# Kernel tuning notes

Measured on AMD Instinct MI355X. Metric: run time of the kernel, lower is better.

Reference implementation:

```python
import jax, jax.numpy as jnp
import numpy as np

N, DIN, DOUT = 8192, 512, 256


def setup_inputs() -> dict:
    key = jax.random.key(0)
    ks = jax.random.split(key, 8)
    s_in = 1.0 / np.sqrt(DIN)   # ~ torch Linear default init scale
    s_out = 1.0 / np.sqrt(DOUT)
    return {
        "x": jax.random.normal(ks[0], (N, DIN), jnp.float32),
        "Wm": jax.random.normal(ks[1], (DIN, DOUT), jnp.float32) * s_in,
        "Wn": jax.random.normal(ks[2], (DIN, DOUT), jnp.float32) * s_in,
        "Wr": jax.random.normal(ks[3], (DIN, DOUT), jnp.float32) * s_in,
        "Wt": jax.random.normal(ks[4], (DIN, DOUT), jnp.float32) * s_in,
        "Wrg": jax.random.normal(ks[5], (DOUT, DOUT), jnp.float32) * s_out,
        "brg": jnp.zeros((DOUT,), jnp.float32),
        "Wlg": jax.random.normal(ks[6], (DOUT, DOUT), jnp.float32) * s_out,
        "blg": jnp.zeros((DOUT,), jnp.float32),
        "Wp": jax.random.normal(ks[7], (DOUT, 1), jnp.float32) * s_out,
        "bp": jnp.zeros((1,), jnp.float32),
    }


def reference(x, Wm, Wn, Wr, Wt, Wrg, brg, Wlg, blg, Wp, bp):
    n = x.shape[0]
    xm = x @ Wm                      # [N, 256]
    xn = x @ Wn                      # [N, 256]
    # pairwise Euclidean distance via GEMM trick (avoids O(N^2*D) diff tensor)
    sq = (jnp.sum(xm * xm, axis=-1)[:, None]
          + jnp.sum(xn * xn, axis=-1)[None, :]
          - 2.0 * (xm @ xn.T))       # [N, N]
    dist = jnp.sqrt(jnp.maximum(sq, 0.0)) * 0.5
    exps = jnp.exp(-dist) / (n / 64.0)
    eye = jnp.eye(n, dtype=x.dtype)
    adj = exps * (1.0 - eye) + eye   # unit diagonal, scaled off-diagonal
    xr = adj @ (x @ Wr)              # graph conv: [N,N]@[N,256]
    xl = x @ Wt
    w = jax.nn.sigmoid(xr @ Wrg + brg + xl @ Wlg + blg)
    feat = (1.0 - w) * xr + w * xl   # gated fusion
    score = feat @ Wp + bp           # [N, 1]
    return adj, score
```

## Files before the change

### kernel.cpp

```cpp
#include <hip/hip_runtime.h>
#include <stdint.h>

typedef __attribute__((ext_vector_type(8))) short bf16x8;
typedef __attribute__((ext_vector_type(4))) float f32x4;

__device__ __forceinline__ unsigned short f2bf(float f){
  unsigned u = __float_as_uint(f);
  u += 0x7FFFu + ((u >> 16) & 1u);
  return (unsigned short)(u >> 16);
}
__device__ __forceinline__ float bf2f(unsigned short s){
  return __uint_as_float(((unsigned)s) << 16);
}

__device__ __forceinline__ int lds_off(int r, int b){
  return r * 128 + (b ^ ((r & 7) << 4));
}

template<int ROWS, int NT>
__device__ __forceinline__ void stage_bf16(unsigned short* lds, const unsigned short* g,
                                           long row0, long stride, long k0, int tid){
#pragma unroll
  for (int c = tid; c < ROWS * 8; c += NT){
    int r = c >> 3, s = c & 7;
    uint4 v = *(const uint4*)(g + (row0 + r) * stride + k0 + s * 8);
    *(uint4*)((char*)lds + lds_off(r, s * 16)) = v;
  }
}

template<int ROWS, int NT>
__device__ __forceinline__ void stage_f32(unsigned short* lds, const float* g,
                                          long row0, long stride, long k0, int tid){
#pragma unroll
  for (int c = tid; c < ROWS * 8; c += NT){
    int r = c >> 3, s = c & 7;
    const float* src = g + (row0 + r) * stride + k0 + s * 8;
    float4 v0 = *(const float4*)(src);
    float4 v1 = *(const float4*)(src + 4);
    unsigned short t[8] = { f2bf(v0.x), f2bf(v0.y), f2bf(v0.z), f2bf(v0.w),
                            f2bf(v1.x), f2bf(v1.y), f2bf(v1.z), f2bf(v1.w) };
    *(uint4*)((char*)lds + lds_off(r, s * 16)) = *(const uint4*)t;
  }
}

__device__ __forceinline__ void mfma_chunk(const unsigned short* ldsA, const unsigned short* ldsB,
                                           int wm, int wn, int lane, f32x4 acc[4][4]){
  int r = lane & 15, gq = lane >> 4;
#pragma unroll
  for (int ks = 0; ks < 2; ++ks){
    bf16x8 a[4], b[4];
    int bb = ks * 64 + gq * 16;
#pragma unroll
    for (int m = 0; m < 4; ++m)
      a[m] = *(const bf16x8*)((const char*)ldsA + lds_off(wm * 64 + m * 16 + r, bb));
#pragma unroll
    for (int n = 0; n < 4; ++n)
      b[n] = *(const bf16x8*)((const char*)ldsB + lds_off(wn * 64 + n * 16 + r, bb));
#pragma unroll
    for (int m = 0; m < 4; ++m)
#pragma unroll
      for (int n = 0; n < 4; ++n)
        acc[m][n] = __builtin_amdgcn_mfma_f32_16x16x32_bf16(a[m], b[n], acc[m][n], 0, 0, 0);
  }
}

__global__ __launch_bounds__(256) void k_prep(const float* Wm, const float* Wn,
    const float* Wr, const float* Wt, const float* Wrg, const float* Wlg, const float* bp,
    unsigned short* WT, unsigned short* WcatT, float* score){
  long id = (long)blockIdx.x * 256 + threadIdx.x;
  if (id < 1024L * 512){
    int n = (int)(id >> 9), k = (int)(id & 511);
    const float* W = (n < 256) ? Wm : ((n < 512) ? Wn : ((n < 768) ? Wr : Wt));
    WT[id] = f2bf(W[(long)k * 256 + (n & 255)]);
  }
  if (id < 256L * 512){
    int n = (int)(id >> 9), k = (int)(id & 511);
    WcatT[id] = f2bf(k < 256 ? Wrg[(long)k * 256 + n] : Wlg[(long)(k - 256) * 256 + n]);
  }
  if (id < 8192) score[id] = bp[0];
}

__global__ __launch_bounds__(256) void k_gemmA(const float* x, const unsigned short* WT,
    unsigned short* xm, unsigned short* xn, unsigned short* xwrT, unsigned short* xl){
  __shared__ unsigned short ldsA[128 * 64];
  __shared__ unsigned short ldsB[128 * 64];
  int tid = threadIdx.x, lane = tid & 63, w = tid >> 6;
  int wm = w >> 1, wn = w & 1;
  int bm = blockIdx.x, bn = blockIdx.y;
  f32x4 acc[4][4];
  f32x4 zero = {0.f, 0.f, 0.f, 0.f};
#pragma unroll
  for (int m = 0; m < 4; ++m)
#pragma unroll
    for (int n = 0; n < 4; ++n) acc[m][n] = zero;

  for (int k0 = 0; k0 < 512; k0 += 64){
    __syncthreads();
    stage_f32<128, 256>(ldsA, x, (long)bm * 128, 512, k0, tid);
    stage_bf16<128, 256>(ldsB, WT, (long)bn * 128, 512, k0, tid);
    __syncthreads();
    mfma_chunk(ldsA, ldsB, wm, wn, lane, acc);
  }
  int r = lane & 15, gq = lane >> 4;
  int i0 = bm * 128 + wm * 64;
  int n0 = bn * 128 + wn * 64;
#pragma unroll
  for (int m = 0; m < 4; ++m){
#pragma unroll
    for (int n = 0; n < 4; ++n){
      int ng = n0 + n * 16 + r;
      int sector = ng >> 8, nc = ng & 255;
      int ib = i0 + m * 16 + gq * 4;
      if (sector == 2){
        unsigned short p[4];
#pragma unroll
        for (int q = 0; q < 4; ++q) p[q] = f2bf(acc[m][n][q]);
        *(uint2*)(xwrT + (long)nc * 8192 + ib) =
            make_uint2((unsigned)p[0] | ((unsigned)p[1] << 16),
                       (unsigned)p[2] | ((unsigned)p[3] << 16));
      } else {
        unsigned short* dst = sector == 0 ? xm : (sector == 1 ? xn : xl);
#pragma unroll
        for (int q = 0; q < 4; ++q)
          dst[(long)(ib + q) * 256 + nc] = f2bf(acc[m][n][q]);
      }
    }
  }
}

__global__ __launch_bounds__(256) void k_norms(const unsigned short* xm, const unsigned short* xn,
                                               float* nm, float* nn){
  int w = threadIdx.x >> 6, lane = threadIdx.x & 63;
  int row = blockIdx.x * 4 + w;
  const unsigned short* src = (row < 8192) ? xm : xn;
  int rr = row & 8191;
  unsigned short v[4];
  *(uint2*)v = *(const uint2*)(src + (long)rr * 256 + lane * 4);
  float s = 0.f;
#pragma unroll
  for (int t = 0; t < 4; ++t){ float f = bf2f(v[t]); s += f * f; }
#pragma unroll
  for (int o = 32; o; o >>= 1) s += __shfl_xor(s, o);
  if (lane == 0) ((row < 8192) ? nm : nn)[rr] = s;
}

__global__ __launch_bounds__(256) void k_adj(const unsigned short* xm, const unsigned short* xn,
                                             const float* nm, const float* nn, float* adj){
  __shared__ unsigned short ldsA[128 * 64];
  __shared__ unsigned short ldsB[128 * 64];
  int tid = threadIdx.x, lane = tid & 63, w = tid >> 6;
  int wm = w >> 1, wn = w & 1;
  int bm = blockIdx.x, bn = blockIdx.y;
  f32x4 acc[4][4];
  f32x4 zero = {0.f, 0.f, 0.f, 0.f};
#pragma unroll
  for (int m = 0; m < 4; ++m)
#pragma unroll
    for (int n = 0; n < 4; ++n) acc[m][n] = zero;

  for (int k0 = 0; k0 < 256; k0 += 64){
    __syncthreads();
    stage_bf16<128, 256>(ldsA, xm, (long)bm * 128, 256, k0, tid);
    stage_bf16<128, 256>(ldsB, xn, (long)bn * 128, 256, k0, tid);
    __syncthreads();
    mfma_chunk(ldsA, ldsB, wm, wn, lane, acc);
  }
  int r = lane & 15, gq = lane >> 4;
#pragma unroll
  for (int m = 0; m < 4; ++m){
#pragma unroll
    for (int n = 0; n < 4; ++n){
      long j = (long)bn * 128 + wn * 64 + n * 16 + r;
      float nnj = nn[j];
#pragma unroll
      for (int q = 0; q < 4; ++q){
        long i = (long)bm * 128 + wm * 64 + m * 16 + gq * 4 + q;
        float sq = nm[i] + nnj - 2.f * acc[m][n][q];
        float d = sqrtf(fmaxf(sq, 0.f)) * 0.5f;
        float e = __expf(-d) * (1.f / 128.f);
        adj[i * 8192 + j] = (i == j) ? 1.f : e;
      }
    }
  }
}

__global__ __launch_bounds__(512) void k_xr(const float* adj, const unsigned short* xwrT,
                                            float* partial, int klen){
  __shared__ unsigned short ldsA[128 * 64];
  __shared__ unsigned short ldsB[256 * 64];
  int tid = threadIdx.x, lane = tid & 63, w = tid >> 6;
  int wm = w >> 2, wn = w & 3;
  int bm = blockIdx.x, sp = blockIdx.y;
  long j0 = (long)sp * klen;
  f32x4 acc[4][4];
  f32x4 zero = {0.f, 0.f, 0.f, 0.f};
#pragma unroll
  for (int m = 0; m < 4; ++m)
#pragma unroll
    for (int n = 0; n < 4; ++n) acc[m][n] = zero;

  for (int k0 = 0; k0 < klen; k0 += 64){
    __syncthreads();
    stage_f32<128, 512>(ldsA, adj, (long)bm * 128, 8192, j0 + k0, tid);
    stage_bf16<256, 512>(ldsB, xwrT, 0, 8192, j0 + k0, tid);
    __syncthreads();
    mfma_chunk(ldsA, ldsB, wm, wn, lane, acc);
  }
  int r = lane & 15, gq = lane >> 4;
  float* dst = partial + (long)sp * 8192 * 256;
#pragma unroll
  for (int m = 0; m < 4; ++m){
#pragma unroll
    for (int n = 0; n < 4; ++n){
      int c = wn * 64 + n * 16 + r;
#pragma unroll
      for (int q = 0; q < 4; ++q){
        long i = (long)bm * 128 + wm * 64 + m * 16 + gq * 4 + q;
        dst[i * 256 + c] = acc[m][n][q];
      }
    }
  }
}

__global__ __launch_bounds__(256) void k_reduce_xr(const float* partial, unsigned short* xr, int S){
  long idx = ((long)blockIdx.x * 256 + threadIdx.x) * 4;
  float4 a = *(const float4*)(partial + idx);
  for (int s = 1; s < S; ++s){
    const float4 b = *(const float4*)(partial + (long)s * 8192 * 256 + idx);
    a.x += b.x; a.y += b.y; a.z += b.z; a.w += b.w;
  }
  unsigned short p[4] = { f2bf(a.x), f2bf(a.y), f2bf(a.z), f2bf(a.w) };
  *(uint2*)(xr + idx) = make_uint2((unsigned)p[0] | ((unsigned)p[1] << 16),
                                   (unsigned)p[2] | ((unsigned)p[3] << 16));
}

__global__ __launch_bounds__(512) void k_gate(const unsigned short* xr, const unsigned short* xl,
    const unsigned short* WcatT, const float* brg, const float* blg,
    const float* Wp, float* score){
  __shared__ unsigned short ldsA[128 * 64];
  __shared__ unsigned short ldsB[256 * 64];
  int tid = threadIdx.x, lane = tid & 63, w = tid >> 6;
  int wm = w >> 2, wn = w & 3;
  int bm = blockIdx.x;
  f32x4 acc[4][4];
  f32x4 zero = {0.f, 0.f, 0.f, 0.f};
#pragma unroll
  for (int m = 0; m < 4; ++m)
#pragma unroll
    for (int n = 0; n < 4; ++n) acc[m][n] = zero;

  for (int k0 = 0; k0 < 512; k0 += 64){
    const unsigned short* A = (k0 < 256) ? xr : xl;
    __syncthreads();
    stage_bf16<128, 512>(ldsA, A, (long)bm * 128, 256, k0 & 255, tid);
    stage_bf16<256, 512>(ldsB, WcatT, 0, 512, k0, tid);
    __syncthreads();
    mfma_chunk(ldsA, ldsB, wm, wn, lane, acc);
  }
  int r = lane & 15, gq = lane >> 4;
#pragma unroll
  for (int m = 0; m < 4; ++m){
#pragma unroll
    for (int q = 0; q < 4; ++q){
      long i = (long)bm * 128 + wm * 64 + m * 16 + gq * 4 + q;
      float part = 0.f;
#pragma unroll
      for (int n = 0; n < 4; ++n){
        int c = wn * 64 + n * 16 + r;
        float arg = acc[m][n][q] + brg[c] + blg[c];
        float wv = 1.f / (1.f + __expf(-arg));
        float xrv = bf2f(xr[i * 256 + c]);
        float xlv = bf2f(xl[i * 256 + c]);
        float feat = (1.f - wv) * xrv + wv * xlv;
        part += feat * Wp[c];
      }
      part += __shfl_xor(part, 1);
      part += __shfl_xor(part, 2);
      part += __shfl_xor(part, 4);
      part += __shfl_xor(part, 8);
      if (r == 0) atomicAdd(score + i, part);
    }
  }
}

extern "C" void kernel_launch(void* const* d_in, const int* in_sizes, int n_in,
                              void* d_out, int out_size, void* d_ws, size_t ws_size,
                              hipStream_t stream){
  const float* x   = (const float*)d_in[0];
  const float* Wm  = (const float*)d_in[1];
  const float* Wn  = (const float*)d_in[2];
  const float* Wr  = (const float*)d_in[3];
  const float* Wt  = (const float*)d_in[4];
  const float* Wrg = (const float*)d_in[5];
  const float* brg = (const float*)d_in[6];
  const float* Wlg = (const float*)d_in[7];
  const float* blg = (const float*)d_in[8];
  const float* Wp  = (const float*)d_in[9];
  const float* bp  = (const float*)d_in[10];

  float* adj   = (float*)d_out;
  float* score = adj + 8192L * 8192;

  char* wsb = (char*)d_ws;
  unsigned short* xm    = (unsigned short*)(wsb);
  unsigned short* xn    = (unsigned short*)(wsb + (4L  << 20));
  unsigned short* xwrT  = (unsigned short*)(wsb + (8L  << 20));
  unsigned short* xl    = (unsigned short*)(wsb + (12L << 20));
  unsigned short* xr    = (unsigned short*)(wsb + (16L << 20));
  float*          nm    = (float*)         (wsb + (20L << 20));
  float*          nn    = nm + 8192;
  unsigned short* WT    = (unsigned short*)(wsb + (21L << 20));
  unsigned short* WcatT = (unsigned short*)(wsb + (22L << 20));
  float*          partial = (float*)(wsb + (23L << 20));

  int S = 1;
  size_t base = 23L << 20;
  if      (ws_size >= base + 4 * (8L << 20)) S = 4;
  else if (ws_size >= base + 2 * (8L << 20)) S = 2;

  k_prep  <<<2048, 256, 0, stream>>>(Wm, Wn, Wr, Wt, Wrg, Wlg, bp, WT, WcatT, score);
  k_gemmA <<<dim3(64, 8), 256, 0, stream>>>(x, WT, xm, xn, xwrT, xl);
  k_norms <<<4096, 256, 0, stream>>>(xm, xn, nm, nn);
  k_adj   <<<dim3(64, 64), 256, 0, stream>>>(xm, xn, nm, nn, adj);
  k_xr    <<<dim3(64, S), 512, 0, stream>>>(adj, xwrT, partial, 8192 / S);
  k_reduce_xr<<<2048, 256, 0, stream>>>(partial, xr, S);
  k_gate  <<<64, 512, 0, stream>>>(xr, xl, WcatT, brg, blg, Wp, score);
}
```

Baseline: 323.3 us.

## Fuse adjacency generation with adj@XWr GEMM to avoid rereading adj

Merges the adjacency kernel and the graph-conv GEMM into one kernel. Each block owns a 128-row strip, generates adjacency tiles, writes them to global memory and keeps a bf16 copy in LDS that feeds the second GEMM directly, so the 256MB fp32 adj matrix is never read back. The cost is a grid of at most 64×4 blocks instead of 4096, which lowers parallelism and latency hiding, and each block repeatedly restages the same xm strip.

```diff
diff --git a/kernel.cpp b/kernel.cpp
--- a/kernel.cpp
+++ b/kernel.cpp
@@ -15,6 +15,9 @@
 
 __device__ __forceinline__ int lds_off(int r, int b){
   return r * 128 + (b ^ ((r & 7) << 4));
+}
+__device__ __forceinline__ int ldsP_off(int r, int b){
+  return r * 256 + (b ^ ((r & 7) << 4));
 }
 
 template<int ROWS, int NT>
@@ -144,79 +147,119 @@
   if (lane == 0) ((row < 8192) ? nm : nn)[rr] = s;
 }
 
-__global__ __launch_bounds__(256) void k_adj(const unsigned short* xm, const unsigned short* xn,
-                                             const float* nm, const float* nn, float* adj){
-  __shared__ unsigned short ldsA[128 * 64];
-  __shared__ unsigned short ldsB[128 * 64];
+__global__ __launch_bounds__(512, 2) void k_adj_xr(
+    const unsigned short* xm, const unsigned short* xn,
+    const float* nm, const float* nn, const unsigned short* xwrT,
+    float* adj, float* partial, int ntiles){
+  __shared__ char smem[65536];
+  unsigned short* ldsA  = (unsigned short*)smem;
+  unsigned short* ldsB  = (unsigned short*)(smem + 16384);
+  unsigned short* ldsB2 = (unsigned short*)smem;
+  char*           ldsP  = smem + 32768;
+
   int tid = threadIdx.x, lane = tid & 63, w = tid >> 6;
-  int wm = w >> 1, wn = w & 1;
-  int bm = blockIdx.x, bn = blockIdx.y;
-  f32x4 acc[4][4];
+  int r = lane & 15, gq = lane >> 4;
+  int wm = w >> 2, wq = w & 3;
+  int bm = blockIdx.x, sp = blockIdx.y;
+
   f32x4 zero = {0.f, 0.f, 0.f, 0.f};
+  f32x4 acc2[4][4];
 #pragma unroll
   for (int m = 0; m < 4; ++m)
 #pragma unroll
-    for (int n = 0; n < 4; ++n) acc[m][n] = zero;
-
-  for (int k0 = 0; k0 < 256; k0 += 64){
-    __syncthreads();
-    stage_bf16<128, 256>(ldsA, xm, (long)bm * 128, 256, k0, tid);
-    stage_bf16<128, 256>(ldsB, xn, (long)bn * 128, 256, k0, tid);
-    __syncthreads();
-    mfma_chunk(ldsA, ldsB, wm, wn, lane, acc);
-  }
-  int r = lane & 15, gq = lane >> 4;
+    for (int n = 0; n < 4; ++n) acc2[m][n] = zero;
+
+  float nmr[4][4];
+#pragma unroll
+  for (int m = 0; m < 4; ++m)
+#pragma unroll
+    for (int q = 0; q < 4; ++q)
+      nmr[m][q] = nm[bm * 128 + wm * 64 + m * 16 + gq * 4 + q];
+
+  for (int t = 0; t < ntiles; ++t){
+    int bn = sp * ntiles + t;
+    f32x4 acc1[4][2];
+#pragma unroll
+    for (int m = 0; m < 4; ++m)
+#pragma unroll
+      for (int n = 0; n < 2; ++n) acc1[m][n] = zero;
+
+    for (int k0 = 0; k0 < 256; k0 += 64){
+      __syncthreads();
+      stage_bf16<128, 512>(ldsA, xm, (long)bm * 128, 256, k0, tid);
+      stage_bf16<128, 512>(ldsB, xn, (long)bn * 128, 256, k0, tid);
+      __syncthreads();
+#pragma unroll
+      for (int ks = 0; ks < 2; ++ks){
+        int bb = ks * 64 + gq * 16;
+        bf16x8 a[4], b[2];
+#pragma unroll
+        for (int m = 0; m < 4; ++m)
+          a[m] = *(const bf16x8*)((const char*)ldsA + lds_off(wm * 64 + m * 16 + r, bb));
+#pragma unroll
+        for (int n = 0; n < 2; ++n)
+          b[n] = *(const bf16x8*)((const char*)ldsB + lds_off(wq * 32 + n * 16 + r, bb));
+#pragma unroll
+        for (int m = 0; m < 4; ++m)
+#pragma unroll
+          for (int n = 0; n < 2; ++n)
+            acc1[m][n] = __builtin_amdgcn_mfma_f32_16x16x32_bf16(a[m], b[n], acc1[m][n], 0, 0, 0);
+      }
+    }
+
+#pragma unroll
+    for (int n = 0; n < 2; ++n){
+      int jl = wq * 32 + n * 16 + r;
+      long j = (long)bn * 128 + jl;
+      float nnj = nn[j];
+#pragma unroll
+      for (int m = 0; m < 4; ++m){
+#pragma unroll
+        for (int q = 0; q < 4; ++q){
+          int il = wm * 64 + m * 16 + gq * 4 + q;
+          long i = (long)bm * 128 + il;
+          float sq = nmr[m][q] + nnj - 2.f * acc1[m][n][q];
+          float d = sqrtf(fmaxf(sq, 0.f)) * 0.5f;
+          float v = (i == j) ? 1.f : __expf(-d) * (1.f / 128.f);
+          adj[i * 8192 + j] = v;
+          *(unsigned short*)(ldsP + ldsP_off(il, jl * 2)) = f2bf(v);
+        }
+      }
+    }
+
+    for (int k0 = 0; k0 < 128; k0 += 64){
+      __syncthreads();
+      stage_bf16<256, 512>(ldsB2, xwrT, 0, 8192, (long)bn * 128 + k0, tid);
+      __syncthreads();
+#pragma unroll
+      for (int ks = 0; ks < 2; ++ks){
+        int kk = k0 + ks * 32;
+        bf16x8 a[4], b[4];
+#pragma unroll
+        for (int m = 0; m < 4; ++m)
+          a[m] = *(const bf16x8*)(ldsP + ldsP_off(wm * 64 + m * 16 + r, kk * 2 + gq * 16));
+#pragma unroll
+        for (int n = 0; n < 4; ++n)
+          b[n] = *(const bf16x8*)((const char*)ldsB2 + lds_off(wq * 64 + n * 16 + r, ks * 64 + gq * 16));
+#pragma unroll
+        for (int m = 0; m < 4; ++m)
+#pragma unroll
+          for (int n = 0; n < 4; ++n)
+            acc2[m][n] = __builtin_amdgcn_mfma_f32_16x16x32_bf16(a[m], b[n], acc2[m][n], 0, 0, 0);
+      }
+    }
+  }
+
+  float* dst = partial + (long)sp * 8192 * 256;
 #pragma unroll
   for (int m = 0; m < 4; ++m){
 #pragma unroll
     for (int n = 0; n < 4; ++n){
-      long j = (long)bn * 128 + wn * 64 + n * 16 + r;
-      float nnj = nn[j];
+      int c = wq * 64 + n * 16 + r;
 #pragma unroll
       for (int q = 0; q < 4; ++q){
         long i = (long)bm * 128 + wm * 64 + m * 16 + gq * 4 + q;
-        float sq = nm[i] + nnj - 2.f * acc[m][n][q];
-        float d = sqrtf(fmaxf(sq, 0.f)) * 0.5f;
-        float e = __expf(-d) * (1.f / 128.f);
-        adj[i * 8192 + j] = (i == j) ? 1.f : e;
-      }
-    }
-  }
-}
-
-__global__ __launch_bounds__(512) void k_xr(const float* adj, const unsigned short* xwrT,
-                                            float* partial, int klen){
-  __shared__ unsigned short ldsA[128 * 64];
-  __shared__ unsigned short ldsB[256 * 64];
-  int tid = threadIdx.x, lane = tid & 63, w = tid >> 6;
-  int wm = w >> 2, wn = w & 3;
-  int bm = blockIdx.x, sp = blockIdx.y;
-  long j0 = (long)sp * klen;
-  f32x4 acc[4][4];
-  f32x4 zero = {0.f, 0.f, 0.f, 0.f};
-#pragma unroll
-  for (int m = 0; m < 4; ++m)
-#pragma unroll
-    for (int n = 0; n < 4; ++n) acc[m][n] = zero;
-
-  for (int k0 = 0; k0 < klen; k0 += 64){
-    __syncthreads();
-    stage_f32<128, 512>(ldsA, adj, (long)bm * 128, 8192, j0 + k0, tid);
-    stage_bf16<256, 512>(ldsB, xwrT, 0, 8192, j0 + k0, tid);
-    __syncthreads();
-    mfma_chunk(ldsA, ldsB, wm, wn, lane, acc);
-  }
-  int r = lane & 15, gq = lane >> 4;
-  float* dst = partial + (long)sp * 8192 * 256;
-#pragma unroll
-  for (int m = 0; m < 4; ++m){
-#pragma unroll
-    for (int n = 0; n < 4; ++n){
-      int c = wn * 64 + n * 16 + r;
-#pragma unroll
-      for (int q = 0; q < 4; ++q){
-        long i = (long)bm * 128 + wm * 64 + m * 16 + gq * 4 + q;
-        dst[i * 256 + c] = acc[m][n][q];
+        dst[i * 256 + c] = acc2[m][n][q];
       }
     }
   }
@@ -313,16 +356,15 @@
   unsigned short* WcatT = (unsigned short*)(wsb + (22L << 20));
   float*          partial = (float*)(wsb + (23L << 20));
 
-  int S = 1;
+  int NS = 1;
   size_t base = 23L << 20;
-  if      (ws_size >= base + 4 * (8L << 20)) S = 4;
-  else if (ws_size >= base + 2 * (8L << 20)) S = 2;
+  if      (ws_size >= base + 4 * (8L << 20)) NS = 4;
+  else if (ws_size >= base + 2 * (8L << 20)) NS = 2;
 
   k_prep  <<<2048, 256, 0, stream>>>(Wm, Wn, Wr, Wt, Wrg, Wlg, bp, WT, WcatT, score);
   k_gemmA <<<dim3(64, 8), 256, 0, stream>>>(x, WT, xm, xn, xwrT, xl);
   k_norms <<<4096, 256, 0, stream>>>(xm, xn, nm, nn);
-  k_adj   <<<dim3(64, 64), 256, 0, stream>>>(xm, xn, nm, nn, adj);
-  k_xr    <<<dim3(64, S), 512, 0, stream>>>(adj, xwrT, partial, 8192 / S);
-  k_reduce_xr<<<2048, 256, 0, stream>>>(partial, xr, S);
+  k_adj_xr<<<dim3(64, NS), 512, 0, stream>>>(xm, xn, nm, nn, xwrT, adj, partial, 64 / NS);
+  k_reduce_xr<<<2048, 256, 0, stream>>>(partial, xr, NS);
   k_gate  <<<64, 512, 0, stream>>>(xr, xl, WcatT, brg, blg, Wp, score);
 }
```

After: 378.0 us. 16.9% more time.
